# Performance work log

Hardware: AMD Instinct MI355X
Metric: run time of the kernel (lower is better)

Reference implementation:

```python
import jax, jax.numpy as jnp
import numpy as np

B, S, E, H, V = 128, 400, 512, 512, 50000


def setup_inputs() -> dict:
    key = jax.random.key(0)
    ks = jax.random.split(key, 16)
    s = 0.05  # param scale
    return {
        "embedded": jax.random.normal(ks[0], (B, E), jnp.float32),
        "hidden": jax.random.normal(ks[1], (1, B, H), jnp.float32),
        "encoder_states": jax.random.normal(ks[2], (S, B, H), jnp.float32),
        "encoder_word_idx": jax.random.randint(ks[3], (S, B), 0, V),
        "ext_vocab_size": V,
        "W_ih": jax.random.normal(ks[4], (3 * H, E), jnp.float32) * s,
        "W_hh": jax.random.normal(ks[5], (3 * H, H), jnp.float32) * s,
        "b_ih": jax.random.normal(ks[6], (3 * H,), jnp.float32) * s,
        "b_hh": jax.random.normal(ks[7], (3 * H,), jnp.float32) * s,
        "W_bil": jax.random.normal(ks[8], (1, H, H), jnp.float32) * s,
        "b_bil": jax.random.normal(ks[9], (1,), jnp.float32) * s,
        "W_out": jax.random.normal(ks[10], (V, 2 * H), jnp.float32) * s,
        "b_out": jax.random.normal(ks[11], (V,), jnp.float32) * s,
        "W_ptr": jax.random.normal(ks[12], (1, 2 * H), jnp.float32) * s,
        "b_ptr": jax.random.normal(ks[13], (1,), jnp.float32) * s,
    }


def reference(embedded, hidden, encoder_states, encoder_word_idx, ext_vocab_size,
              W_ih, W_hh, b_ih, b_hh, W_bil, b_bil, W_out, b_out, W_ptr, b_ptr):
    h = hidden[0]  # [B, H]
    # --- single-step GRU (PyTorch gate order r, z, n) ---
    gi = embedded @ W_ih.T + b_ih          # [B, 3H]
    gh = h @ W_hh.T + b_hh                 # [B, 3H]
    i_r, i_z, i_n = jnp.split(gi, 3, axis=1)
    h_r, h_z, h_n = jnp.split(gh, 3, axis=1)
    r = jax.nn.sigmoid(i_r + h_r)
    z = jax.nn.sigmoid(i_z + h_z)
    n = jnp.tanh(i_n + r * h_n)
    h_new = (1.0 - z) * n + z * h          # [B, H]
    # --- bilinear attention energy over src dim ---
    # hidden is broadcast along S, so precompute h_new @ W once.
    v = h_new @ W_bil[0]                                   # [B, H]
    energy = jnp.einsum('bh,sbh->sb', v, encoder_states) + b_bil[0]  # [S, B]
    attn = jax.nn.softmax(energy, axis=0)                  # softmax over src len
    context = jnp.einsum('sbh,sb->bh', encoder_states, attn)  # [B, H]
    combined = jnp.concatenate([h_new, context], axis=1)   # [B, 2H]
    # --- output assembly: generator softmax + pointer mix ---
    logits = combined @ W_out.T + b_out                    # [B, V]
    prob_ptr = jax.nn.sigmoid(combined @ W_ptr.T + b_ptr)  # [B, 1]
    gen = jax.nn.softmax(logits, axis=1)
    Bsz = embedded.shape[0]
    out = jnp.zeros((Bsz, ext_vocab_size), logits.dtype)
    out = out.at[:, :logits.shape[1]].set((1.0 - prob_ptr) * gen)
    idx = encoder_word_idx.T                               # [B, S]
    out = out.at[jnp.arange(Bsz)[:, None], idx].add(prob_ptr * attn.T)
    out = jnp.log(out)                                     # log_prob=True
    enc_attn = attn.T[:, :, None]                          # [B, S, 1]
    return out, h_new[None], enc_attn, prob_ptr
```

## Files before the change

### kernel.cpp

```cpp
#include <hip/hip_runtime.h>
#include <cstdint>
#include <cstddef>

typedef float f4 __attribute__((ext_vector_type(4)));
typedef float f2 __attribute__((ext_vector_type(2)));
typedef short short8 __attribute__((ext_vector_type(8)));

#define NB 128
#define NH 512
#define NS 400
#define NV 50000
#define NEGBIG (-3.402823466e38f)

__device__ __forceinline__ unsigned short f2bf(float f) {
  unsigned u = __float_as_uint(f);
  u = u + 0x7fffu + ((u >> 16) & 1u);
  return (unsigned short)(u >> 16);
}

__device__ __forceinline__ int fragidx(int m, int k) {
  int c = k >> 7;
  int t = (k >> 5) & 3;
  int q = (k >> 3) & 3;
  int o = k & 7;
  return ((((c * 4 + t) * 8 + (m >> 4)) * 64) + q * 16 + (m & 15)) * 8 + o;
}

__global__ __launch_bounds__(256) void k1_gigh(
    const float* __restrict__ emb, const float* __restrict__ hid,
    const float* __restrict__ Wih, const float* __restrict__ Whh,
    float* __restrict__ C)
{
  __shared__ float As[32 * 68];
  __shared__ float Bs[32 * 36];
  const int tid = threadIdx.x;
  const int n0g = blockIdx.x * 32;
  const int m0  = blockIdx.y * 64;
  const float* A; const float* Bm; int n0;
  if (n0g < 1536) { A = emb; Bm = Wih; n0 = n0g; }
  else            { A = hid; Bm = Whh; n0 = n0g - 1536; }
  const int mt = tid & 15, nt = tid >> 4;
  const int arow = tid >> 2, ac = tid & 3;
  const int brow = tid >> 3, bc = tid & 7;
  float acc[4][2] = {};
  for (int k0 = 0; k0 < 512; k0 += 32) {
    f4 x0 = *(const f4*)(A + (m0 + arow) * 512 + k0 + ac * 8);
    f4 x1 = *(const f4*)(A + (m0 + arow) * 512 + k0 + ac * 8 + 4);
    f4 y  = *(const f4*)(Bm + (n0 + brow) * 512 + k0 + bc * 4);
    __syncthreads();
#pragma unroll
    for (int kk = 0; kk < 4; kk++) {
      As[(ac * 8 + kk) * 68 + arow]     = x0[kk];
      As[(ac * 8 + 4 + kk) * 68 + arow] = x1[kk];
      Bs[(bc * 4 + kk) * 36 + brow]     = y[kk];
    }
    __syncthreads();
#pragma unroll
    for (int kk = 0; kk < 32; kk++) {
      f4 a = *(const f4*)(As + kk * 68 + mt * 4);
      f2 b = *(const f2*)(Bs + kk * 36 + nt * 2);
#pragma unroll
      for (int i = 0; i < 4; i++) {
        acc[i][0] += a[i] * b[0];
        acc[i][1] += a[i] * b[1];
      }
    }
  }
#pragma unroll
  for (int i = 0; i < 4; i++) {
    f2 o; o[0] = acc[i][0]; o[1] = acc[i][1];
    *(f2*)(C + (size_t)(m0 + mt * 4 + i) * 3072 + n0g + nt * 2) = o;
  }
}

__global__ __launch_bounds__(256) void k2_gates(
    const float* __restrict__ gigh, const float* __restrict__ hid,
    const float* __restrict__ bih, const float* __restrict__ bhh,
    float* __restrict__ out_h, float* __restrict__ comb,
    unsigned short* __restrict__ cbf)
{
  int i = blockIdx.x * 256 + threadIdx.x;
  int b = i >> 9, j = i & 511;
  const float* gg = gigh + b * 3072;
  float ir  = gg[j]        + bih[j];
  float iz  = gg[j + 512]  + bih[j + 512];
  float in_ = gg[j + 1024] + bih[j + 1024];
  float hr  = gg[j + 1536] + bhh[j];
  float hz  = gg[j + 2048] + bhh[j + 512];
  float hn  = gg[j + 2560] + bhh[j + 1024];
  float r = 1.f / (1.f + expf(-(ir + hr)));
  float z = 1.f / (1.f + expf(-(iz + hz)));
  float n = tanhf(in_ + r * hn);
  float hnew = (1.f - z) * n + z * hid[i];
  out_h[i] = hnew;
  comb[b * 1024 + j] = hnew;
  cbf[fragidx(b, j)] = f2bf(hnew);
}

__global__ __launch_bounds__(256) void k3_v(
    const float* __restrict__ comb, const float* __restrict__ Wbil,
    float* __restrict__ v)
{
  int i = blockIdx.x * 256 + threadIdx.x;
  int b = i >> 9, j = i & 511;
  const float* x = comb + b * 1024;
  float acc = 0.f;
#pragma unroll 16
  for (int h = 0; h < 512; h++) acc += x[h] * Wbil[h * 512 + j];
  v[i] = acc;
}

__global__ __launch_bounds__(128) void k4_energy(
    const float* __restrict__ enc, const float* __restrict__ v,
    const float* __restrict__ bbil, float* __restrict__ energy)
{
  int tid = threadIdx.x;
  int wid = tid >> 6, lane = tid & 63;
  int b = blockIdx.y;
  int sc = blockIdx.x * 2 + wid;
  const float* vr = v + b * 512 + lane * 8;
  f4 v0 = *(const f4*)vr, v1 = *(const f4*)(vr + 4);
  float e[8];
#pragma unroll
  for (int i = 0; i < 8; i++) {
    int s = sc * 8 + i;
    const float* er = enc + ((size_t)(s * 128 + b)) * 512 + lane * 8;
    f4 e0 = *(const f4*)er, e1 = *(const f4*)(er + 4);
    e[i] = e0[0]*v0[0] + e0[1]*v0[1] + e0[2]*v0[2] + e0[3]*v0[3]
         + e1[0]*v1[0] + e1[1]*v1[1] + e1[2]*v1[2] + e1[3]*v1[3];
  }
#pragma unroll
  for (int i = 0; i < 8; i++)
#pragma unroll
    for (int o = 32; o; o >>= 1) e[i] += __shfl_xor(e[i], o);
  if (lane == 0) {
    float bb = bbil[0];
    f4 o0, o1;
    o0[0] = e[0] + bb; o0[1] = e[1] + bb; o0[2] = e[2] + bb; o0[3] = e[3] + bb;
    o1[0] = e[4] + bb; o1[1] = e[5] + bb; o1[2] = e[6] + bb; o1[3] = e[7] + bb;
    *(f4*)(energy + b * 400 + sc * 8)     = o0;
    *(f4*)(energy + b * 400 + sc * 8 + 4) = o1;
  }
}

__global__ __launch_bounds__(256) void k4_softmax(
    float* __restrict__ energy, float* __restrict__ out_attn)
{
  __shared__ float sm[4];
  int b = blockIdx.x, tid = threadIdx.x;
  float* e = energy + b * 400;
  float e0 = (tid < 400)       ? e[tid]       : NEGBIG;
  float e1 = (tid + 256 < 400) ? e[tid + 256] : NEGBIG;
  float m = fmaxf(e0, e1);
#pragma unroll
  for (int o = 32; o; o >>= 1) m = fmaxf(m, __shfl_xor(m, o));
  if ((tid & 63) == 0) sm[tid >> 6] = m;
  __syncthreads();
  m = fmaxf(fmaxf(sm[0], sm[1]), fmaxf(sm[2], sm[3]));
  __syncthreads();
  float x0 = (tid < 400)       ? expf(e0 - m) : 0.f;
  float x1 = (tid + 256 < 400) ? expf(e1 - m) : 0.f;
  float s = x0 + x1;
#pragma unroll
  for (int o = 32; o; o >>= 1) s += __shfl_xor(s, o);
  if ((tid & 63) == 0) sm[tid >> 6] = s;
  __syncthreads();
  s = sm[0] + sm[1] + sm[2] + sm[3];
  float inv = 1.f / s;
  if (tid < 400)       { float a = x0 * inv; e[tid] = a;       out_attn[b * 400 + tid] = a; }
  if (tid + 256 < 400) { float a = x1 * inv; e[tid + 256] = a; out_attn[b * 400 + tid + 256] = a; }
}

__global__ __launch_bounds__(256) void k4_context(
    const float* __restrict__ enc, const float* __restrict__ attn,
    float* __restrict__ P)
{
  __shared__ float at[100];
  int b = blockIdx.y, ht = blockIdx.x & 1, sq = blockIdx.x >> 1;
  int tid = threadIdx.x;
  if (tid < 100) at[tid] = attn[b * 400 + sq * 100 + tid];
  __syncthreads();
  int h = ht * 256 + tid;
  const float* ep = enc + (size_t)(sq * 100 * 128 + b) * 512 + h;
  float acc = 0.f;
#pragma unroll 10
  for (int s = 0; s < 100; s++) acc += at[s] * ep[(size_t)s * 65536];
  P[(size_t)((sq * 128 + b) * 2 + ht) * 256 + tid] = acc;
}

__global__ __launch_bounds__(256) void k4_ctxsum(
    const float* __restrict__ P, float* __restrict__ comb,
    unsigned short* __restrict__ cbf)
{
  int i = blockIdx.x * 256 + threadIdx.x;
  int b = i >> 9, j = i & 511;
  int ht = j >> 8, tt = j & 255;
  float s = 0.f;
#pragma unroll
  for (int q = 0; q < 4; q++) s += P[(size_t)((q * 128 + b) * 2 + ht) * 256 + tt];
  comb[b * 1024 + 512 + j] = s;
  cbf[fragidx(b, 512 + j)] = f2bf(s);
}

__global__ __launch_bounds__(64) void k_pptr(
    const float* __restrict__ comb, const float* __restrict__ Wptr,
    const float* __restrict__ bptr, float* __restrict__ out_p,
    float* __restrict__ p)
{
  int b = blockIdx.x, lane = threadIdx.x;
  const float* x = comb + b * 1024;
  float d = 0.f;
#pragma unroll
  for (int i = 0; i < 16; i++) d += x[i * 64 + lane] * Wptr[i * 64 + lane];
#pragma unroll
  for (int o = 32; o; o >>= 1) d += __shfl_xor(d, o);
  if (lane == 0) {
    float pv = 1.f / (1.f + expf(-(d + bptr[0])));
    out_p[b] = pv;
    p[b] = pv;
  }
}

__global__ __launch_bounds__(128, 2) void k5_logits(
    const unsigned short* __restrict__ Abf, const float* __restrict__ W,
    const float* __restrict__ bout, float* __restrict__ out,
    float* __restrict__ pMS)
{
  __shared__ __align__(16) unsigned short As[16384];
  const int tid = threadIdx.x;
  const int wid = tid >> 6, lane = tid & 63;
  const int quad = lane >> 4, l16 = lane & 15;
  const int vb = blockIdx.x * 64 + wid * 32;
  const int v0 = vb + l16;
  const int v1 = vb + 16 + l16;
  const bool ok0 = v0 < NV, ok1 = v1 < NV;
  const size_t r0 = (size_t)(ok0 ? v0 : NV - 1) * 1024 + quad * 8;
  const size_t r1 = (size_t)(ok1 ? v1 : NV - 1) * 1024 + quad * 8;
  f4 acc0[8] = {}, acc1[8] = {};
  f4 w0[8], w1[8];
#pragma unroll
  for (int t = 0; t < 4; t++) {
    w0[2*t]   = *(const f4*)(W + r0 + t * 32);
    w0[2*t+1] = *(const f4*)(W + r0 + t * 32 + 4);
    w1[2*t]   = *(const f4*)(W + r1 + t * 32);
    w1[2*t+1] = *(const f4*)(W + r1 + t * 32 + 4);
  }
  for (int c = 0; c < 8; c++) {
    const f4* src = (const f4*)(Abf + c * 16384);
    f4* dst = (f4*)As;
    f4 st[16];
#pragma unroll
    for (int j = 0; j < 16; j++) st[j] = src[j * 128 + tid];
    __syncthreads();
#pragma unroll
    for (int j = 0; j < 16; j++) dst[j * 128 + tid] = st[j];
    short8 B0[4], B1[4];
#pragma unroll
    for (int t = 0; t < 4; t++) {
      f4 a = w0[2*t], b = w0[2*t+1], cfl = w1[2*t], d = w1[2*t+1];
      B0[t][0] = (short)f2bf(a[0]); B0[t][1] = (short)f2bf(a[1]);
      B0[t][2] = (short)f2bf(a[2]); B0[t][3] = (short)f2bf(a[3]);
      B0[t][4] = (short)f2bf(b[0]); B0[t][5] = (short)f2bf(b[1]);
      B0[t][6] = (short)f2bf(b[2]); B0[t][7] = (short)f2bf(b[3]);
      B1[t][0] = (short)f2bf(cfl[0]); B1[t][1] = (short)f2bf(cfl[1]);
      B1[t][2] = (short)f2bf(cfl[2]); B1[t][3] = (short)f2bf(cfl[3]);
      B1[t][4] = (short)f2bf(d[0]); B1[t][5] = (short)f2bf(d[1]);
      B1[t][6] = (short)f2bf(d[2]); B1[t][7] = (short)f2bf(d[3]);
    }
    if (c < 7) {
      const float* p0 = W + r0 + (c + 1) * 128;
      const float* p1 = W + r1 + (c + 1) * 128;
#pragma unroll
      for (int t = 0; t < 4; t++) {
        w0[2*t]   = *(const f4*)(p0 + t * 32);
        w0[2*t+1] = *(const f4*)(p0 + t * 32 + 4);
        w1[2*t]   = *(const f4*)(p1 + t * 32);
        w1[2*t+1] = *(const f4*)(p1 + t * 32 + 4);
      }
    }
    __syncthreads();
#pragma unroll
    for (int t = 0; t < 4; t++) {
      const short8* afp = (const short8*)(As + t * 4096);
#pragma unroll
      for (int mt = 0; mt < 8; mt++) {
        short8 af = afp[mt * 64 + lane];
        acc0[mt] = __builtin_amdgcn_mfma_f32_16x16x32_bf16(af, B0[t], acc0[mt], 0, 0, 0);
        acc1[mt] = __builtin_amdgcn_mfma_f32_16x16x32_bf16(af, B1[t], acc1[mt], 0, 0, 0);
      }
    }
  }
  float bias0 = ok0 ? bout[v0] : 0.f;
  float bias1 = ok1 ? bout[v1] : 0.f;
#pragma unroll
  for (int mt = 0; mt < 8; mt++) {
#pragma unroll
    for (int r = 0; r < 4; r++) {
      int brow = mt * 16 + quad * 4 + r;
      float a0 = ok0 ? acc0[mt][r] + bias0 : NEGBIG;
      float a1 = ok1 ? acc1[mt][r] + bias1 : NEGBIG;
      if (ok0) out[(size_t)brow * NV + v0] = a0;
      if (ok1) out[(size_t)brow * NV + v1] = a1;
      float m = fmaxf(a0, a1);
#pragma unroll
      for (int o = 8; o; o >>= 1) m = fmaxf(m, __shfl_xor(m, o));
      float s = (ok0 ? expf(a0 - m) : 0.f) + (ok1 ? expf(a1 - m) : 0.f);
#pragma unroll
      for (int o = 8; o; o >>= 1) s += __shfl_xor(s, o);
      if (l16 == 0) {
        f2 ms; ms[0] = m; ms[1] = s;
        *(f2*)(pMS + (size_t)brow * 3200 + (blockIdx.x * 2 + wid) * 2) = ms;
      }
    }
  }
}

__global__ __launch_bounds__(256) void k5_reduce(
    const float* __restrict__ pMS, const float* __restrict__ p,
    float* __restrict__ t)
{
  __shared__ float sm[4];
  int b = blockIdx.x, tid = threadIdx.x;
  const f2* q = (const f2*)(pMS + (size_t)b * 3200);
  float M = NEGBIG;
  for (int i = tid; i < 1564; i += 256) M = fmaxf(M, q[i][0]);
#pragma unroll
  for (int o = 32; o; o >>= 1) M = fmaxf(M, __shfl_xor(M, o));
  if ((tid & 63) == 0) sm[tid >> 6] = M;
  __syncthreads();
  M = fmaxf(fmaxf(sm[0], sm[1]), fmaxf(sm[2], sm[3]));
  __syncthreads();
  float S = 0.f;
  for (int i = tid; i < 1564; i += 256) {
    f2 v = q[i];
    S += v[1] * expf(v[0] - M);
  }
#pragma unroll
  for (int o = 32; o; o >>= 1) S += __shfl_xor(S, o);
  if ((tid & 63) == 0) sm[tid >> 6] = S;
  __syncthreads();
  if (tid == 0) {
    float Sf = sm[0] + sm[1] + sm[2] + sm[3];
    t[b] = -M - logf(Sf) + logf(1.f - p[b]);
  }
}

__global__ __launch_bounds__(256) void k5_shift(
    float* __restrict__ out, const float* __restrict__ t)
{
  int vv = blockIdx.x * 256 + threadIdx.x;
  int b = blockIdx.y;
  if (vv < NV) out[(size_t)b * NV + vv] += t[b];
}

__global__ __launch_bounds__(256) void k5_scatter(
    const int* __restrict__ idx, const float* __restrict__ p,
    const float* __restrict__ attn, float* __restrict__ out)
{
  int i = blockIdx.x * 256 + threadIdx.x;
  if (i >= NS * NB) return;
  int s = i >> 7, b = i & 127;
  float add = p[b] * attn[b * 400 + s];
  int* ai = (int*)(out + (size_t)b * NV + idx[i]);
  int cur = *ai;
  while (true) {
    float oldf = __int_as_float(cur);
    float nv = logf(expf(oldf) + add);
    int got = atomicCAS(ai, cur, __float_as_int(nv));
    if (got == cur) break;
    cur = got;
  }
}

extern "C" void kernel_launch(void* const* d_in, const int* in_sizes, int n_in,
                              void* d_out, int out_size, void* d_ws, size_t ws_size,
                              hipStream_t stream) {
  (void)in_sizes; (void)n_in; (void)out_size; (void)ws_size;
  const float* emb  = (const float*)d_in[0];
  const float* hid  = (const float*)d_in[1];
  const float* enc  = (const float*)d_in[2];
  const int*   widx = (const int*)d_in[3];
  const float* Wih  = (const float*)d_in[5];
  const float* Whh  = (const float*)d_in[6];
  const float* bih  = (const float*)d_in[7];
  const float* bhh  = (const float*)d_in[8];
  const float* Wbil = (const float*)d_in[9];
  const float* bbil = (const float*)d_in[10];
  const float* Wout = (const float*)d_in[11];
  const float* bout = (const float*)d_in[12];
  const float* Wptr = (const float*)d_in[13];
  const float* bptr = (const float*)d_in[14];

  float* out      = (float*)d_out;
  float* out_logp = out;
  float* out_h    = out + 6400000;
  float* out_attn = out + 6465536;
  float* out_p    = out + 6516736;

  float* ws   = (float*)d_ws;
  float* gigh = ws;
  float* comb = ws + 393216;
  float* vws  = ws + 524288;
  float* attn = ws + 589824;
  float* pws  = ws + 641024;
  float* tws  = ws + 641152;
  unsigned short* cbf = (unsigned short*)(ws + 641280);
  float* Pctx = ws + 706816;
  float* pMS  = ws + 968960;

  k1_gigh   <<<dim3(96, 2),    256, 0, stream>>>(emb, hid, Wih, Whh, gigh);
  k2_gates  <<<256,            256, 0, stream>>>(gigh, hid, bih, bhh, out_h, comb, cbf);
  k3_v      <<<256,            256, 0, stream>>>(comb, Wbil, vws);
  k4_energy <<<dim3(25, 128),  128, 0, stream>>>(enc, vws, bbil, attn);
  k4_softmax<<<128,            256, 0, stream>>>(attn, out_attn);
  k4_context<<<dim3(8, 128),   256, 0, stream>>>(enc, attn, Pctx);
  k4_ctxsum <<<256,            256, 0, stream>>>(Pctx, comb, cbf);
  k_pptr    <<<128,             64, 0, stream>>>(comb, Wptr, bptr, out_p, pws);
  k5_logits <<<782,            128, 0, stream>>>(cbf, Wout, bout, out_logp, pMS);
  k5_reduce <<<128,            256, 0, stream>>>(pMS, pws, tws);
  k5_shift  <<<dim3(196, 128), 256, 0, stream>>>(out_logp, tws);
  k5_scatter<<<200,            256, 0, stream>>>(widx, pws, attn, out_logp);
}
```

Baseline: 508.5 us.

## Fuse softmax into context, ctxsum with pointer gate, reduce with shift; async LDS loads

Softmax over the source dimension is recomputed inside each context block instead of running as its own kernel. The context partial-sum reduction is merged with the pointer-gate dot product, and the logsumexp reduction is merged with the log-prob shift. The logits kernel now stages the activation tile with global_load_lds direct-to-LDS copies, and a barrier is moved. Together these cut the launch count from 12 to 9 and remove the register staging, at the cost of redundant softmax and reduction work per block.

```diff
diff --git a/kernel.cpp b/kernel.cpp
--- a/kernel.cpp
+++ b/kernel.cpp
@@ -16,6 +16,12 @@
   unsigned u = __float_as_uint(f);
   u = u + 0x7fffu + ((u >> 16) & 1u);
   return (unsigned short)(u >> 16);
+}
+
+__device__ __forceinline__ void load_lds16(const f4* g, f4* l) {
+  __builtin_amdgcn_global_load_lds(
+      (const __attribute__((address_space(1))) unsigned int*)g,
+      (__attribute__((address_space(3))) unsigned int*)l, 16, 0, 0);
 }
 
 __device__ __forceinline__ int fragidx(int m, int k) {
@@ -143,42 +149,35 @@
   }
 }
 
-__global__ __launch_bounds__(256) void k4_softmax(
-    float* __restrict__ energy, float* __restrict__ out_attn)
+__global__ __launch_bounds__(256) void k4_ctx(
+    const float* __restrict__ enc, const float* __restrict__ energy,
+    float* __restrict__ out_attn, float* __restrict__ P)
 {
   __shared__ float sm[4];
-  int b = blockIdx.x, tid = threadIdx.x;
-  float* e = energy + b * 400;
-  float e0 = (tid < 400)       ? e[tid]       : NEGBIG;
-  float e1 = (tid + 256 < 400) ? e[tid + 256] : NEGBIG;
-  float m = fmaxf(e0, e1);
-#pragma unroll
-  for (int o = 32; o; o >>= 1) m = fmaxf(m, __shfl_xor(m, o));
-  if ((tid & 63) == 0) sm[tid >> 6] = m;
-  __syncthreads();
-  m = fmaxf(fmaxf(sm[0], sm[1]), fmaxf(sm[2], sm[3]));
-  __syncthreads();
-  float x0 = (tid < 400)       ? expf(e0 - m) : 0.f;
-  float x1 = (tid + 256 < 400) ? expf(e1 - m) : 0.f;
-  float s = x0 + x1;
-#pragma unroll
-  for (int o = 32; o; o >>= 1) s += __shfl_xor(s, o);
-  if ((tid & 63) == 0) sm[tid >> 6] = s;
-  __syncthreads();
-  s = sm[0] + sm[1] + sm[2] + sm[3];
-  float inv = 1.f / s;
-  if (tid < 400)       { float a = x0 * inv; e[tid] = a;       out_attn[b * 400 + tid] = a; }
-  if (tid + 256 < 400) { float a = x1 * inv; e[tid + 256] = a; out_attn[b * 400 + tid + 256] = a; }
-}
-
-__global__ __launch_bounds__(256) void k4_context(
-    const float* __restrict__ enc, const float* __restrict__ attn,
-    float* __restrict__ P)
-{
   __shared__ float at[100];
   int b = blockIdx.y, ht = blockIdx.x & 1, sq = blockIdx.x >> 1;
   int tid = threadIdx.x;
-  if (tid < 100) at[tid] = attn[b * 400 + sq * 100 + tid];
+  const float* E = energy + b * 400;
+  float e0 = E[tid];
+  float e1 = (tid + 256 < 400) ? E[tid + 256] : NEGBIG;
+  float m = fmaxf(e0, e1);
+#pragma unroll
+  for (int o = 32; o; o >>= 1) m = fmaxf(m, __shfl_xor(m, o));
+  if ((tid & 63) == 0) sm[tid >> 6] = m;
+  __syncthreads();
+  m = fmaxf(fmaxf(sm[0], sm[1]), fmaxf(sm[2], sm[3]));
+  __syncthreads();
+  float x = expf(e0 - m) + ((tid + 256 < 400) ? expf(e1 - m) : 0.f);
+#pragma unroll
+  for (int o = 32; o; o >>= 1) x += __shfl_xor(x, o);
+  if ((tid & 63) == 0) sm[tid >> 6] = x;
+  __syncthreads();
+  float invS = 1.f / (sm[0] + sm[1] + sm[2] + sm[3]);
+  if (tid < 100) {
+    float a = expf(E[sq * 100 + tid] - m) * invS;
+    at[tid] = a;
+    if (ht == 0) out_attn[b * 400 + sq * 100 + tid] = a;
+  }
   __syncthreads();
   int h = ht * 256 + tid;
   const float* ep = enc + (size_t)(sq * 100 * 128 + b) * 512 + h;
@@ -188,36 +187,36 @@
   P[(size_t)((sq * 128 + b) * 2 + ht) * 256 + tid] = acc;
 }
 
-__global__ __launch_bounds__(256) void k4_ctxsum(
-    const float* __restrict__ P, float* __restrict__ comb,
-    unsigned short* __restrict__ cbf)
-{
-  int i = blockIdx.x * 256 + threadIdx.x;
-  int b = i >> 9, j = i & 511;
-  int ht = j >> 8, tt = j & 255;
-  float s = 0.f;
-#pragma unroll
-  for (int q = 0; q < 4; q++) s += P[(size_t)((q * 128 + b) * 2 + ht) * 256 + tt];
-  comb[b * 1024 + 512 + j] = s;
-  cbf[fragidx(b, 512 + j)] = f2bf(s);
-}
-
-__global__ __launch_bounds__(64) void k_pptr(
-    const float* __restrict__ comb, const float* __restrict__ Wptr,
-    const float* __restrict__ bptr, float* __restrict__ out_p,
-    float* __restrict__ p)
-{
-  int b = blockIdx.x, lane = threadIdx.x;
-  const float* x = comb + b * 1024;
-  float d = 0.f;
-#pragma unroll
-  for (int i = 0; i < 16; i++) d += x[i * 64 + lane] * Wptr[i * 64 + lane];
-#pragma unroll
-  for (int o = 32; o; o >>= 1) d += __shfl_xor(d, o);
-  if (lane == 0) {
+__global__ __launch_bounds__(256) void k4_cp(
+    const float* __restrict__ P, const float* __restrict__ comb_in,
+    const float* __restrict__ Wptr, const float* __restrict__ bptr,
+    float* __restrict__ comb, unsigned short* __restrict__ cbf,
+    float* __restrict__ out_p, float* __restrict__ pw)
+{
+  __shared__ float sm[4];
+  int b = blockIdx.x, tid = threadIdx.x;
+  float dot = 0.f;
+#pragma unroll
+  for (int half = 0; half < 2; half++) {
+    int j = tid + half * 256;
+    int ht = j >> 8, tt = j & 255;
+    float s = 0.f;
+#pragma unroll
+    for (int q = 0; q < 4; q++) s += P[(size_t)((q * 128 + b) * 2 + ht) * 256 + tt];
+    comb[b * 1024 + 512 + j] = s;
+    cbf[fragidx(b, 512 + j)] = f2bf(s);
+    dot += s * Wptr[512 + j];
+    dot += comb_in[b * 1024 + j] * Wptr[j];
+  }
+#pragma unroll
+  for (int o = 32; o; o >>= 1) dot += __shfl_xor(dot, o);
+  if ((tid & 63) == 0) sm[tid >> 6] = dot;
+  __syncthreads();
+  if (tid == 0) {
+    float d = sm[0] + sm[1] + sm[2] + sm[3];
     float pv = 1.f / (1.f + expf(-(d + bptr[0])));
     out_p[b] = pv;
-    p[b] = pv;
+    pw[b] = pv;
   }
 }
 
@@ -248,12 +247,9 @@
   for (int c = 0; c < 8; c++) {
     const f4* src = (const f4*)(Abf + c * 16384);
     f4* dst = (f4*)As;
-    f4 st[16];
-#pragma unroll
-    for (int j = 0; j < 16; j++) st[j] = src[j * 128 + tid];
     __syncthreads();
 #pragma unroll
-    for (int j = 0; j < 16; j++) dst[j * 128 + tid] = st[j];
+    for (int j = 0; j < 16; j++) load_lds16(src + j * 128 + tid, dst + j * 128 + tid);
     short8 B0[4], B1[4];
 #pragma unroll
     for (int t = 0; t < 4; t++) {
@@ -267,6 +263,7 @@
       B1[t][4] = (short)f2bf(d[0]); B1[t][5] = (short)f2bf(d[1]);
       B1[t][6] = (short)f2bf(d[2]); B1[t][7] = (short)f2bf(d[3]);
     }
+    __syncthreads();
     if (c < 7) {
       const float* p0 = W + r0 + (c + 1) * 128;
       const float* p1 = W + r1 + (c + 1) * 128;
@@ -278,7 +275,6 @@
         w1[2*t+1] = *(const f4*)(p1 + t * 32 + 4);
       }
     }
-    __syncthreads();
 #pragma unroll
     for (int t = 0; t < 4; t++) {
       const short8* afp = (const short8*)(As + t * 4096);
@@ -315,12 +311,12 @@
   }
 }
 
-__global__ __launch_bounds__(256) void k5_reduce(
-    const float* __restrict__ pMS, const float* __restrict__ p,
-    float* __restrict__ t)
+__global__ __launch_bounds__(256) void k5_shift(
+    float* __restrict__ out, const float* __restrict__ pMS,
+    const float* __restrict__ p)
 {
   __shared__ float sm[4];
-  int b = blockIdx.x, tid = threadIdx.x;
+  int b = blockIdx.y, seg = blockIdx.x, tid = threadIdx.x;
   const f2* q = (const f2*)(pMS + (size_t)b * 3200);
   float M = NEGBIG;
   for (int i = tid; i < 1564; i += 256) M = fmaxf(M, q[i][0]);
@@ -339,18 +335,9 @@
   for (int o = 32; o; o >>= 1) S += __shfl_xor(S, o);
   if ((tid & 63) == 0) sm[tid >> 6] = S;
   __syncthreads();
-  if (tid == 0) {
-    float Sf = sm[0] + sm[1] + sm[2] + sm[3];
-    t[b] = -M - logf(Sf) + logf(1.f - p[b]);
-  }
-}
-
-__global__ __launch_bounds__(256) void k5_shift(
-    float* __restrict__ out, const float* __restrict__ t)
-{
-  int vv = blockIdx.x * 256 + threadIdx.x;
-  int b = blockIdx.y;
-  if (vv < NV) out[(size_t)b * NV + vv] += t[b];
+  float t = -M - logf(sm[0] + sm[1] + sm[2] + sm[3]) + logf(1.f - p[b]);
+  float* o = out + (size_t)b * NV + seg * 6250;
+  for (int i = tid; i < 6250; i += 256) o[i] += t;
 }
 
 __global__ __launch_bounds__(256) void k5_scatter(
@@ -397,27 +384,23 @@
   float* out_attn = out + 6465536;
   float* out_p    = out + 6516736;
 
-  float* ws   = (float*)d_ws;
-  float* gigh = ws;
-  float* comb = ws + 393216;
-  float* vws  = ws + 524288;
-  float* attn = ws + 589824;
-  float* pws  = ws + 641024;
-  float* tws  = ws + 641152;
+  float* ws     = (float*)d_ws;
+  float* gigh   = ws;
+  float* comb   = ws + 393216;
+  float* vws    = ws + 524288;
+  float* energy = ws + 589824;
+  float* pws    = ws + 641024;
   unsigned short* cbf = (unsigned short*)(ws + 641280);
-  float* Pctx = ws + 706816;
-  float* pMS  = ws + 968960;
-
-  k1_gigh   <<<dim3(96, 2),    256, 0, stream>>>(emb, hid, Wih, Whh, gigh);
-  k2_gates  <<<256,            256, 0, stream>>>(gigh, hid, bih, bhh, out_h, comb, cbf);
-  k3_v      <<<256,            256, 0, stream>>>(comb, Wbil, vws);
-  k4_energy <<<dim3(25, 128),  128, 0, stream>>>(enc, vws, bbil, attn);
-  k4_softmax<<<128,            256, 0, stream>>>(attn, out_attn);
-  k4_context<<<dim3(8, 128),   256, 0, stream>>>(enc, attn, Pctx);
-  k4_ctxsum <<<256,            256, 0, stream>>>(Pctx, comb, cbf);
-  k_pptr    <<<128,             64, 0, stream>>>(comb, Wptr, bptr, out_p, pws);
-  k5_logits <<<782,            128, 0, stream>>>(cbf, Wout, bout, out_logp, pMS);
-  k5_reduce <<<128,            256, 0, stream>>>(pMS, pws, tws);
-  k5_shift  <<<dim3(196, 128), 256, 0, stream>>>(out_logp, tws);
-  k5_scatter<<<200,            256, 0, stream>>>(widx, pws, attn, out_logp);
-}
+  float* Pctx   = ws + 706816;
+  float* pMS    = ws + 968960;
+
+  k1_gigh   <<<dim3(96, 2),   256, 0, stream>>>(emb, hid, Wih, Whh, gigh);
+  k2_gates  <<<256,           256, 0, stream>>>(gigh, hid, bih, bhh, out_h, comb, cbf);
+  k3_v      <<<256,           256, 0, stream>>>(comb, Wbil, vws);
+  k4_energy <<<dim3(25, 128), 128, 0, stream>>>(enc, vws, bbil, energy);
+  k4_ctx    <<<dim3(8, 128),  256, 0, stream>>>(enc, energy, out_attn, Pctx);
+  k4_cp     <<<128,           256, 0, stream>>>(Pctx, comb, Wptr, bptr, comb, cbf, out_p, pws);
+  k5_logits <<<782,           128, 0, stream>>>(cbf, Wout, bout, out_logp, pMS);
+  k5_shift  <<<dim3(8, 128),  256, 0, stream>>>(out_logp, pMS, pws);
+  k5_scatter<<<200,           256, 0, stream>>>(widx, pws, out_attn, out_logp);
+}
```

After: 495.0 us. 1.03x faster.
